# Performance work log

Hardware: AMD Instinct MI355X
Metric: run time of the kernel (lower is better)

## Reference

```python
import jax, jax.numpy as jnp
import numpy as np

N_NODES = 20000
N_EDGES = 640000
N_FEATS = 3703
HIDDEN = 50
N_CLASSES = 6
N_KENN_LAYERS = 3
# clause: not C_c(x) OR C_c(y) OR not Cite(x,y)  -> literal signs
SIGNS = np.array([-1.0, 1.0, -1.0], dtype=np.float32)


def setup_inputs() -> dict:
    key = jax.random.key(0)
    ks = jax.random.split(key, 12)
    features = jax.random.normal(ks[0], (N_NODES, N_FEATS), dtype=jnp.float32)
    relations = jax.random.normal(ks[1], (N_EDGES, 1), dtype=jnp.float32)
    sx = jax.random.randint(ks[2], (N_EDGES,), 0, N_NODES)
    sy = jax.random.randint(ks[3], (N_EDGES,), 0, N_NODES)

    def dense(k, fan_in, fan_out):
        return jax.random.normal(k, (fan_in, fan_out), dtype=jnp.float32) / np.sqrt(fan_in).astype(np.float32)

    W1 = dense(ks[4], N_FEATS, HIDDEN); b1 = jnp.zeros((HIDDEN,), jnp.float32)
    W2 = dense(ks[5], HIDDEN, HIDDEN);  b2 = jnp.zeros((HIDDEN,), jnp.float32)
    W3 = dense(ks[6], HIDDEN, HIDDEN);  b3 = jnp.zeros((HIDDEN,), jnp.float32)
    W4 = dense(ks[7], HIDDEN, N_CLASSES); b4 = jnp.zeros((N_CLASSES,), jnp.float32)
    # one learnable clause weight per class-clause, per KENN layer (init 0.5 as in KENN)
    clause_weights = jnp.full((N_KENN_LAYERS, N_CLASSES), 0.5, dtype=jnp.float32)
    return dict(features=features, relations=relations, sx=sx, sy=sy,
                W1=W1, b1=b1, W2=W2, b2=b2, W3=W3, b3=b3, W4=W4, b4=b4,
                clause_weights=clause_weights)


def _kenn_layer(z, relations, sx, sy, cw):
    # z: [N, C]; relations: [E, 1]; cw: [C] clause weights
    n = z.shape[0]
    zx = z[sx]                                   # [E, C] gather head literals
    zy = z[sy]                                   # [E, C] gather tail literals
    rel = jnp.broadcast_to(relations, (relations.shape[0], z.shape[1]))  # [E, C]
    signs = jnp.asarray(SIGNS)
    # signed literal preactivations per clause: [E, C, 3]
    v = jnp.stack([-zx, zy, -rel], axis=-1)
    # KENN boost: delta = w_c * softmax(signed preacts) * sign
    d = cw[None, :, None] * jax.nn.softmax(v, axis=-1) * signs[None, None, :]
    # scatter unary deltas back to nodes (relation delta is discarded)
    dz = jax.ops.segment_sum(d[..., 0], sx, num_segments=n)
    dz = dz + jax.ops.segment_sum(d[..., 1], sy, num_segments=n)
    return z + dz


def reference(features, relations, sx, sy, W1, b1, W2, b2, W3, b3, W4, b4, clause_weights):
    # MLP preactivations (dropout inactive at inference)
    x = jax.nn.relu(features @ W1 + b1)
    x = jax.nn.relu(x @ W2 + b2)
    x = jax.nn.relu(x @ W3 + b3)
    z = x @ W4 + b4                               # [N, 6]
    for i in range(N_KENN_LAYERS):
        z = _kenn_layer(z, relations, sx, sy, clause_weights[i])
    return jax.nn.softmax(z, axis=-1)
```

## Files before the change

### kernel.cpp

```cpp
#include <hip/hip_runtime.h>

#define M_NODES 20000
#define K_FEATS 3703
#define PADK 3712
#define NH 50
#define NC 6
#define N_EDGES_C 640000
#define NKB 116

typedef __attribute__((ext_vector_type(8))) __bf16 bf16x8;
typedef __attribute__((ext_vector_type(4))) float f32x4;

__global__ void k_packB(const float* __restrict__ W1, unsigned short* __restrict__ Bh,
                        unsigned short* __restrict__ Bl) {
  int idx = blockIdx.x * 256 + threadIdx.x;
  if (idx >= NKB * 4 * 64 * 8) return;
  int j = idx & 7;
  int lane = (idx >> 3) & 63;
  int t = (idx >> 9) & 3;
  int kb = idx >> 11;
  int k = kb * 32 + (lane >> 4) * 8 + j;
  int c = t * 16 + (lane & 15);
  float v = (k < K_FEATS && c < NH) ? W1[k * NH + c] : 0.f;
  __bf16 hb = (__bf16)v;
  float hf = (float)hb;
  __bf16 lb = (__bf16)(v - hf);
  Bh[idx] = *(unsigned short*)&hb;
  Bl[idx] = *(unsigned short*)&lb;
}

__global__ __launch_bounds__(256) void k_gemm1(const float* __restrict__ A,
    const unsigned short* __restrict__ Bph, const unsigned short* __restrict__ Bpl,
    float* __restrict__ part, int KS) {
  const int lane = threadIdx.x & 63;
  const int w = threadIdx.x >> 6;
  const int row0 = blockIdx.x * 128 + w * 32;
  const int s = blockIdx.y;
  const int ks = s * KS;
  const int ke = (ks + KS < PADK) ? ks + KS : PADK;
  const int nsteps = (ke - ks) >> 5;
  const int g = lane >> 4;
  const int rl = lane & 15;
  const int r0c = min(row0 + rl, M_NODES - 1);
  const int r1c = min(row0 + 16 + rl, M_NODES - 1);
  const float* a0p = A + (size_t)r0c * K_FEATS + 8 * g;
  const float* a1p = A + (size_t)r1c * K_FEATS + 8 * g;
  const bf16x8* BH = (const bf16x8*)Bph;
  const bf16x8* BL = (const bf16x8*)Bpl;

  f32x4 acc[2][4];
  #pragma unroll
  for (int i = 0; i < 2; ++i)
    #pragma unroll
    for (int t = 0; t < 4; ++t) acc[i][t] = (f32x4){0.f, 0.f, 0.f, 0.f};

  #define LOADA(d0, d1, k0) {                                     \
    d0[0] = *(const float4*)(a0p + (k0));                         \
    d0[1] = *(const float4*)(a0p + (k0) + 4);                     \
    d1[0] = *(const float4*)(a1p + (k0));                         \
    d1[1] = *(const float4*)(a1p + (k0) + 4); }
  #define LOADAG(d0, d1, k0) {                                    \
    _Pragma("unroll") for (int j = 0; j < 8; ++j) {               \
      int gk = (k0) + 8 * g + j;                                  \
      float v0 = (gk < K_FEATS) ? a0p[(k0) + j] : 0.f;            \
      float v1 = (gk < K_FEATS) ? a1p[(k0) + j] : 0.f;            \
      ((float*)d0)[j] = v0; ((float*)d1)[j] = v1; } }

  #define BODY(sa0, sa1, k0) {                                    \
    const int kb4 = ((k0) >> 5) * 4;                              \
    bf16x8 bh0 = BH[(kb4 + 0) * 64 + lane];                       \
    bf16x8 bh1 = BH[(kb4 + 1) * 64 + lane];                       \
    bf16x8 bh2 = BH[(kb4 + 2) * 64 + lane];                       \
    bf16x8 bh3 = BH[(kb4 + 3) * 64 + lane];                       \
    bf16x8 bl0 = BL[(kb4 + 0) * 64 + lane];                       \
    bf16x8 bl1 = BL[(kb4 + 1) * 64 + lane];                       \
    bf16x8 bl2 = BL[(kb4 + 2) * 64 + lane];                       \
    bf16x8 bl3 = BL[(kb4 + 3) * 64 + lane];                       \
    bf16x8 ah0, al0, ah1, al1;                                    \
    _Pragma("unroll") for (int j = 0; j < 8; ++j) {               \
      float xv = ((const float*)sa0)[j];                          \
      __bf16 hb = (__bf16)xv; float hf = (float)hb;               \
      ah0[j] = hb; al0[j] = (__bf16)(xv - hf);                    \
      float yv = ((const float*)sa1)[j];                          \
      __bf16 hb2 = (__bf16)yv; float hf2 = (float)hb2;            \
      ah1[j] = hb2; al1[j] = (__bf16)(yv - hf2);                  \
    }                                                             \
    acc[0][0] = __builtin_amdgcn_mfma_f32_16x16x32_bf16(ah0, bh0, acc[0][0], 0, 0, 0); \
    acc[0][1] = __builtin_amdgcn_mfma_f32_16x16x32_bf16(ah0, bh1, acc[0][1], 0, 0, 0); \
    acc[0][2] = __builtin_amdgcn_mfma_f32_16x16x32_bf16(ah0, bh2, acc[0][2], 0, 0, 0); \
    acc[0][3] = __builtin_amdgcn_mfma_f32_16x16x32_bf16(ah0, bh3, acc[0][3], 0, 0, 0); \
    acc[1][0] = __builtin_amdgcn_mfma_f32_16x16x32_bf16(ah1, bh0, acc[1][0], 0, 0, 0); \
    acc[1][1] = __builtin_amdgcn_mfma_f32_16x16x32_bf16(ah1, bh1, acc[1][1], 0, 0, 0); \
    acc[1][2] = __builtin_amdgcn_mfma_f32_16x16x32_bf16(ah1, bh2, acc[1][2], 0, 0, 0); \
    acc[1][3] = __builtin_amdgcn_mfma_f32_16x16x32_bf16(ah1, bh3, acc[1][3], 0, 0, 0); \
    acc[0][0] = __builtin_amdgcn_mfma_f32_16x16x32_bf16(al0, bh0, acc[0][0], 0, 0, 0); \
    acc[0][1] = __builtin_amdgcn_mfma_f32_16x16x32_bf16(al0, bh1, acc[0][1], 0, 0, 0); \
    acc[0][2] = __builtin_amdgcn_mfma_f32_16x16x32_bf16(al0, bh2, acc[0][2], 0, 0, 0); \
    acc[0][3] = __builtin_amdgcn_mfma_f32_16x16x32_bf16(al0, bh3, acc[0][3], 0, 0, 0); \
    acc[1][0] = __builtin_amdgcn_mfma_f32_16x16x32_bf16(al1, bh0, acc[1][0], 0, 0, 0); \
    acc[1][1] = __builtin_amdgcn_mfma_f32_16x16x32_bf16(al1, bh1, acc[1][1], 0, 0, 0); \
    acc[1][2] = __builtin_amdgcn_mfma_f32_16x16x32_bf16(al1, bh2, acc[1][2], 0, 0, 0); \
    acc[1][3] = __builtin_amdgcn_mfma_f32_16x16x32_bf16(al1, bh3, acc[1][3], 0, 0, 0); \
    acc[0][0] = __builtin_amdgcn_mfma_f32_16x16x32_bf16(ah0, bl0, acc[0][0], 0, 0, 0); \
    acc[0][1] = __builtin_amdgcn_mfma_f32_16x16x32_bf16(ah0, bl1, acc[0][1], 0, 0, 0); \
    acc[0][2] = __builtin_amdgcn_mfma_f32_16x16x32_bf16(ah0, bl2, acc[0][2], 0, 0, 0); \
    acc[0][3] = __builtin_amdgcn_mfma_f32_16x16x32_bf16(ah0, bl3, acc[0][3], 0, 0, 0); \
    acc[1][0] = __builtin_amdgcn_mfma_f32_16x16x32_bf16(ah1, bl0, acc[1][0], 0, 0, 0); \
    acc[1][1] = __builtin_amdgcn_mfma_f32_16x16x32_bf16(ah1, bl1, acc[1][1], 0, 0, 0); \
    acc[1][2] = __builtin_amdgcn_mfma_f32_16x16x32_bf16(ah1, bl2, acc[1][2], 0, 0, 0); \
    acc[1][3] = __builtin_amdgcn_mfma_f32_16x16x32_bf16(ah1, bl3, acc[1][3], 0, 0, 0); }

  float4 xa0[2], xa1[2], ya0[2], ya1[2];
  LOADA(xa0, xa1, ks);
  for (int t2 = 0; t2 < nsteps; t2 += 2) {
    const int k0 = ks + (t2 << 5);
    const int k1 = k0 + 32;
    if (k1 + 32 > K_FEATS) { LOADAG(ya0, ya1, k1); } else { LOADA(ya0, ya1, k1); }
    BODY(xa0, xa1, k0);
    if (t2 + 2 < nsteps) {
      const int k2 = k0 + 64;
      if (k2 + 32 > K_FEATS) { LOADAG(xa0, xa1, k2); } else { LOADA(xa0, xa1, k2); }
    }
    BODY(ya0, ya1, k1);
  }
  #undef LOADA
  #undef LOADAG
  #undef BODY

  float* p = part + (size_t)s * 1000000;
  #pragma unroll
  for (int i = 0; i < 2; ++i) {
    #pragma unroll
    for (int t = 0; t < 4; ++t) {
      int col = t * 16 + rl;
      if (col < NH) {
        int rowb = row0 + i * 16 + g * 4;
        f32x4 v = acc[i][t];
        #pragma unroll
        for (int q = 0; q < 4; ++q) {
          int row = rowb + q;
          if (row < M_NODES) p[row * NH + col] = v[q];
        }
      }
    }
  }
}

__global__ void k_epi(const float* __restrict__ part, const float* __restrict__ b1,
                      float* __restrict__ x1, int S) {
  int i = blockIdx.x * 256 + threadIdx.x;
  if (i >= M_NODES * NH) return;
  float v = b1[i % NH];
  for (int s = 0; s < S; ++s) v += part[(size_t)s * 1000000 + i];
  x1[i] = fmaxf(v, 0.f);
}

__global__ __launch_bounds__(256) void k_mlp(const float* __restrict__ x1,
    const float* __restrict__ W2, const float* __restrict__ b2,
    const float* __restrict__ W3, const float* __restrict__ b3,
    const float* __restrict__ W4, const float* __restrict__ b4,
    float* __restrict__ z) {
  __shared__ float lX[32 * 51];
  __shared__ float lW2[50 * 52];
  __shared__ float lW3[50 * 52];
  __shared__ float lW4[50 * 8];
  const int tid = threadIdx.x;
  const int row0 = blockIdx.x * 32;
  for (int idx = tid; idx < 2500; idx += 256) {
    int k = idx / 50, n = idx % 50;
    lW2[k * 52 + n] = W2[idx];
    lW3[k * 52 + n] = W3[idx];
  }
  for (int idx = tid; idx < 300; idx += 256) {
    int k = idx / 6, n = idx % 6;
    lW4[k * 8 + n] = W4[idx];
  }
  for (int idx = tid; idx < 1600; idx += 256) {
    int r = idx / 50, k = idx % 50;
    int gr = row0 + r;
    lX[r * 51 + k] = (gr < M_NODES) ? x1[gr * 50 + k] : 0.f;
  }
  __syncthreads();
  const int r = tid >> 3, cg = tid & 7;
  float x[50];
  #pragma unroll
  for (int k = 0; k < 50; ++k) x[k] = lX[r * 51 + k];

  for (int layer = 0; layer < 2; ++layer) {
    const float* lW = (layer == 0) ? lW2 : lW3;
    const float* bg = (layer == 0) ? b2 : b3;
    float acc[7];
    #pragma unroll
    for (int j = 0; j < 7; ++j) {
      int n = cg + 8 * j;
      acc[j] = (n < 50) ? bg[n] : 0.f;
    }
    #pragma unroll
    for (int k = 0; k < 50; ++k) {
      float xk = x[k];
      #pragma unroll
      for (int j = 0; j < 7; ++j) {
        int n = cg + 8 * j;
        if (n < 50) acc[j] = fmaf(xk, lW[k * 52 + n], acc[j]);
      }
    }
    __syncthreads();
    #pragma unroll
    for (int j = 0; j < 7; ++j) {
      int n = cg + 8 * j;
      if (n < 50) lX[r * 51 + n] = fmaxf(acc[j], 0.f);
    }
    __syncthreads();
    #pragma unroll
    for (int k = 0; k < 50; ++k) x[k] = lX[r * 51 + k];
  }
  if (cg < 6) {
    float accz = b4[cg];
    #pragma unroll
    for (int k = 0; k < 50; ++k) accz = fmaf(x[k], lW4[k * 8 + cg], accz);
    int gr = row0 + r;
    if (gr < M_NODES) z[gr * 6 + cg] = accz;
  }
}

__global__ void k_count(const int* __restrict__ sx, const int* __restrict__ sy,
                        int* __restrict__ cnt) {
  int e = blockIdx.x * 256 + threadIdx.x;
  if (e >= N_EDGES_C) return;
  atomicAdd(&cnt[sx[e]], 1);
  atomicAdd(&cnt[sy[e]], 1);
}

__global__ __launch_bounds__(1024) void k_scan(const int* __restrict__ cnt,
                                               int* __restrict__ off,
                                               int* __restrict__ cur) {
  __shared__ int sums[1024];
  int t = threadIdx.x;
  int base = t * 20;
  int local[20];
  int s = 0;
  #pragma unroll
  for (int j = 0; j < 20; ++j) {
    int idx = base + j;
    int v = (idx < M_NODES) ? cnt[idx] : 0;
    local[j] = s;
    s += v;
  }
  sums[t] = s;
  __syncthreads();
  for (int d = 1; d < 1024; d <<= 1) {
    int v = (t >= d) ? sums[t - d] : 0;
    __syncthreads();
    sums[t] += v;
    __syncthreads();
  }
  int excl = sums[t] - s;
  #pragma unroll
  for (int j = 0; j < 20; ++j) {
    int idx = base + j;
    if (idx < M_NODES) {
      int o = excl + local[j];
      off[idx] = o;
      cur[idx] = o;
    }
  }
  if (t == 1023) off[M_NODES] = sums[1023];
}

__global__ void k_scatter(const int* __restrict__ sx, const int* __restrict__ sy,
                          const float* __restrict__ rel,
                          int* __restrict__ cur, int2* __restrict__ ent) {
  int e = blockIdx.x * 256 + threadIdx.x;
  if (e >= N_EDGES_C) return;
  int a = sx[e], b = sy[e];
  int rb = __float_as_int(rel[e]);
  int p = atomicAdd(&cur[a], 1);
  ent[p] = make_int2((b << 1), rb);
  int q = atomicAdd(&cur[b], 1);
  ent[q] = make_int2((a << 1) | 1, rb);
}

__global__ __launch_bounds__(256) void k_gather(const float* __restrict__ z,
    const int* __restrict__ off, const int2* __restrict__ ent,
    const float* __restrict__ cw, float* __restrict__ partial) {
  int t = blockIdx.x * 256 + threadIdx.x;
  if (t >= M_NODES * 8) return;
  int s = t & 7;
  int n = t >> 3;
  int o0 = off[n];
  int deg = off[n + 1] - o0;
  int lo = o0 + ((deg * s) >> 3);
  int hi = o0 + ((deg * (s + 1)) >> 3);

  const float2* zr = (const float2*)(z + n * 6);
  float2 a0 = zr[0], a1 = zr[1], a2 = zr[2];
  float znv[6] = {a0.x, a0.y, a1.x, a1.y, a2.x, a2.y};
  float w[6];
  #pragma unroll
  for (int c = 0; c < 6; ++c) w[c] = cw[c];
  float dz[6] = {0.f, 0.f, 0.f, 0.f, 0.f, 0.f};

  for (int i = lo; i < hi; ++i) {
    int2 e2 = ent[i];
    int partner = e2.x >> 1;
    int side = e2.x & 1;
    float r = __int_as_float(e2.y);
    const float2* zp2 = (const float2*)(z + partner * 6);
    float2 p0 = zp2[0], p1 = zp2[1], p2 = zp2[2];
    float zpv[6] = {p0.x, p0.y, p1.x, p1.y, p2.x, p2.y};
    float v2 = -r;
    #pragma unroll
    for (int c = 0; c < 6; ++c) {
      float zx = side ? zpv[c] : znv[c];
      float zy = side ? znv[c] : zpv[c];
      float v0 = -zx, v1 = zy;
      float m = fmaxf(fmaxf(v0, v1), v2);
      float e0 = __expf(v0 - m);
      float e1 = __expf(v1 - m);
      float e2v = __expf(v2 - m);
      float inv = w[c] / (e0 + e1 + e2v);
      dz[c] += (side ? e1 : -e0) * inv;
    }
  }
  float* pp = partial + (size_t)s * 120000 + n * 6;
  #pragma unroll
  for (int c = 0; c < 6; ++c) pp[c] = dz[c];
}

__global__ void k_combine(const float* __restrict__ zc, const float* __restrict__ partial,
                          float* __restrict__ zn) {
  int i = blockIdx.x * 256 + threadIdx.x;
  if (i >= M_NODES * NC) return;
  float v = zc[i];
  #pragma unroll
  for (int s = 0; s < 8; ++s) v += partial[(size_t)s * 120000 + i];
  zn[i] = v;
}

__global__ void k_combine_softmax(const float* __restrict__ zc,
                                  const float* __restrict__ partial,
                                  float* __restrict__ out) {
  int n = blockIdx.x * 256 + threadIdx.x;
  if (n >= M_NODES) return;
  float v[6];
  #pragma unroll
  for (int c = 0; c < 6; ++c) v[c] = zc[n * 6 + c];
  #pragma unroll
  for (int s = 0; s < 8; ++s) {
    const float* pp = partial + (size_t)s * 120000 + n * 6;
    #pragma unroll
    for (int c = 0; c < 6; ++c) v[c] += pp[c];
  }
  float m = v[0];
  #pragma unroll
  for (int c = 1; c < 6; ++c) m = fmaxf(m, v[c]);
  float sum = 0.f, ev[6];
  #pragma unroll
  for (int c = 0; c < 6; ++c) { ev[c] = __expf(v[c] - m); sum += ev[c]; }
  float inv = 1.f / sum;
  float2* o2 = (float2*)(out + n * 6);
  o2[0] = make_float2(ev[0] * inv, ev[1] * inv);
  o2[1] = make_float2(ev[2] * inv, ev[3] * inv);
  o2[2] = make_float2(ev[4] * inv, ev[5] * inv);
}

extern "C" void kernel_launch(void* const* d_in, const int* in_sizes, int n_in,
                              void* d_out, int out_size, void* d_ws, size_t ws_size,
                              hipStream_t stream) {
  const float* A   = (const float*)d_in[0];
  const float* rel = (const float*)d_in[1];
  const int*   sx  = (const int*)d_in[2];
  const int*   sy  = (const int*)d_in[3];
  const float* W1  = (const float*)d_in[4];
  const float* b1  = (const float*)d_in[5];
  const float* W2  = (const float*)d_in[6];
  const float* b2  = (const float*)d_in[7];
  const float* W3  = (const float*)d_in[8];
  const float* b3  = (const float*)d_in[9];
  const float* W4  = (const float*)d_in[10];
  const float* b4  = (const float*)d_in[11];
  const float* cw  = (const float*)d_in[12];

  const int S = 12, KS = 320;

  float* base = (float*)d_ws;
  float* part = base;
  float* x1   = base + 12000000;
  float* zA   = base + 13000000;
  float* zB   = base + 13120000;
  unsigned short* Bph = (unsigned short*)(base + 13240000);
  unsigned short* Bpl = (unsigned short*)(base + 13360000);

  int*  cnt  = (int*)base;
  int*  off  = (int*)base + 24576;
  int*  cur  = (int*)base + 49152;
  int2* ent  = (int2*)((int*)base + 73728);
  float* partial = base + 2700000;

  k_packB<<<(NKB * 4 * 64 * 8 + 255) / 256, 256, 0, stream>>>(W1, Bph, Bpl);
  k_gemm1<<<dim3(157, S), 256, 0, stream>>>(A, Bph, Bpl, part, KS);
  k_epi<<<(M_NODES * NH + 255) / 256, 256, 0, stream>>>(part, b1, x1, S);
  k_mlp<<<(M_NODES + 31) / 32, 256, 0, stream>>>(x1, W2, b2, W3, b3, W4, b4, zA);

  hipMemsetAsync(cnt, 0, (M_NODES + 1) * sizeof(int), stream);
  k_count<<<(N_EDGES_C + 255) / 256, 256, 0, stream>>>(sx, sy, cnt);
  k_scan<<<1, 1024, 0, stream>>>(cnt, off, cur);
  k_scatter<<<(N_EDGES_C + 255) / 256, 256, 0, stream>>>(sx, sy, rel, cur, ent);

  float* zc = zA;
  float* zn = zB;
  for (int l = 0; l < 3; ++l) {
    k_gather<<<(M_NODES * 8 + 255) / 256, 256, 0, stream>>>(zc, off, ent, cw + 6 * l, partial);
    if (l < 2) {
      k_combine<<<(M_NODES * NC + 255) / 256, 256, 0, stream>>>(zc, partial, zn);
      float* t = zc; zc = zn; zn = t;
    } else {
      k_combine_softmax<<<(M_NODES + 255) / 256, 256, 0, stream>>>(zc, partial, (float*)d_out);
    }
  }
}
```

Measured before the change: 359.1 us.

## Deepen GEMM1 A-prefetch to triple buffering and use fewer, longer K splits

The first-layer GEMM loop now keeps three register stages of A tiles in flight instead of two, issuing each load three steps before it is consumed to better hide global-memory latency. The split-K factor drops from 12 to 8 with a longer K slice per split, which cuts partial-sum traffic and the work in the epilogue reduction. The cost is higher register pressure, which may lower occupancy, and fewer blocks (157x8) to spread across the CUs.

```diff
diff --git a/kernel.cpp b/kernel.cpp
--- a/kernel.cpp
+++ b/kernel.cpp
@@ -65,6 +65,9 @@
       float v0 = (gk < K_FEATS) ? a0p[(k0) + j] : 0.f;            \
       float v1 = (gk < K_FEATS) ? a1p[(k0) + j] : 0.f;            \
       ((float*)d0)[j] = v0; ((float*)d1)[j] = v1; } }
+  #define LDSEL(d0, d1, k0) {                                     \
+    if ((k0) + 32 > K_FEATS) { LOADAG(d0, d1, k0) }               \
+    else { LOADA(d0, d1, k0) } }
 
   #define BODY(sa0, sa1, k0) {                                    \
     const int kb4 = ((k0) >> 5) * 4;                              \
@@ -110,32 +113,37 @@
     acc[1][2] = __builtin_amdgcn_mfma_f32_16x16x32_bf16(ah1, bl2, acc[1][2], 0, 0, 0); \
     acc[1][3] = __builtin_amdgcn_mfma_f32_16x16x32_bf16(ah1, bl3, acc[1][3], 0, 0, 0); }
 
-  float4 xa0[2], xa1[2], ya0[2], ya1[2];
-  LOADA(xa0, xa1, ks);
-  for (int t2 = 0; t2 < nsteps; t2 += 2) {
-    const int k0 = ks + (t2 << 5);
-    const int k1 = k0 + 32;
-    if (k1 + 32 > K_FEATS) { LOADAG(ya0, ya1, k1); } else { LOADA(ya0, ya1, k1); }
-    BODY(xa0, xa1, k0);
-    if (t2 + 2 < nsteps) {
-      const int k2 = k0 + 64;
-      if (k2 + 32 > K_FEATS) { LOADAG(xa0, xa1, k2); } else { LOADA(xa0, xa1, k2); }
-    }
-    BODY(ya0, ya1, k1);
-  }
+  float4 p0a[2], p0b[2], p1a[2], p1b[2], p2a[2], p2b[2];
+  LDSEL(p0a, p0b, ks);
+  if (nsteps > 1) LDSEL(p1a, p1b, ks + 32);
+  if (nsteps > 2) LDSEL(p2a, p2b, ks + 64);
+
+  int t = 0;
+  for (; t + 3 <= nsteps; t += 3) {
+    const int k0 = ks + (t << 5);
+    BODY(p0a, p0b, k0);
+    if (t + 3 < nsteps) LDSEL(p0a, p0b, k0 + 96);
+    BODY(p1a, p1b, k0 + 32);
+    if (t + 4 < nsteps) LDSEL(p1a, p1b, k0 + 128);
+    BODY(p2a, p2b, k0 + 64);
+    if (t + 5 < nsteps) LDSEL(p2a, p2b, k0 + 160);
+  }
+  if (t < nsteps)     BODY(p0a, p0b, ks + (t << 5));
+  if (t + 1 < nsteps) BODY(p1a, p1b, ks + ((t + 1) << 5));
   #undef LOADA
   #undef LOADAG
+  #undef LDSEL
   #undef BODY
 
   float* p = part + (size_t)s * 1000000;
   #pragma unroll
   for (int i = 0; i < 2; ++i) {
     #pragma unroll
-    for (int t = 0; t < 4; ++t) {
-      int col = t * 16 + rl;
+    for (int t2 = 0; t2 < 4; ++t2) {
+      int col = t2 * 16 + rl;
       if (col < NH) {
         int rowb = row0 + i * 16 + g * 4;
-        f32x4 v = acc[i][t];
+        f32x4 v = acc[i][t2];
         #pragma unroll
         for (int q = 0; q < 4; ++q) {
           int row = rowb + q;
@@ -381,15 +389,15 @@
   const float* b4  = (const float*)d_in[11];
   const float* cw  = (const float*)d_in[12];
 
-  const int S = 12, KS = 320;
+  const int S = 8, KS = 512;
 
   float* base = (float*)d_ws;
   float* part = base;
-  float* x1   = base + 12000000;
-  float* zA   = base + 13000000;
-  float* zB   = base + 13120000;
-  unsigned short* Bph = (unsigned short*)(base + 13240000);
-  unsigned short* Bpl = (unsigned short*)(base + 13360000);
+  float* x1   = base + 8000000;
+  float* zA   = base + 9000000;
+  float* zB   = base + 9120000;
+  unsigned short* Bph = (unsigned short*)(base + 9240000);
+  unsigned short* Bpl = (unsigned short*)(base + 9360000);
 
   int*  cnt  = (int*)base;
   int*  off  = (int*)base + 24576;
```

After: 356.9 us. About the same (-0.6%).
